# Optimization experiments

Hardware: AMD Instinct MI355X
Metric: run time of the kernel (lower is better)

The kernel has to match this reference:

```python
import jax, jax.numpy as jnp
import numpy as np

B, S, D, H = 8, 2048, 1024, 1024

def setup_inputs() -> dict:
    key = jax.random.key(0)
    ks = jax.random.split(key, 7)
    scale = 1.0 / np.sqrt(D)
    x = jax.random.normal(ks[0], (B, S, D), dtype=jnp.float32)
    W_q = jax.random.uniform(ks[1], (H, D), jnp.float32, -scale, scale)
    b_q = jax.random.uniform(ks[2], (H,), jnp.float32, -scale, scale)
    W_k = jax.random.uniform(ks[3], (H, D), jnp.float32, -scale, scale)
    b_k = jax.random.uniform(ks[4], (H,), jnp.float32, -scale, scale)
    W_v = jax.random.uniform(ks[5], (H, D), jnp.float32, -scale, scale)
    b_v = jax.random.uniform(ks[6], (H,), jnp.float32, -scale, scale)
    return {"x": x, "W_q": W_q, "b_q": b_q, "W_k": W_k, "b_k": b_k, "W_v": W_v, "b_v": b_v}

def reference(x, W_q, b_q, W_k, b_k, W_v, b_v):
    # Linear layers: y = x @ W.T + b (torch nn.Linear convention)
    q = jnp.einsum('bsd,hd->bsh', x, W_q) + b_q
    k = jnp.einsum('bsd,hd->bsh', x, W_k) + b_k
    v = jnp.einsum('bsd,hd->bsh', x, W_v) + b_v
    score = jnp.einsum('bqh,bkh->bqk', q, k) / jnp.sqrt(jnp.float32(H))
    causal = jnp.tril(jnp.ones((S, S), dtype=bool))  # lower-triangular mask
    score = jnp.where(causal, score, jnp.float32(-1e9))
    attn = jax.nn.softmax(score, axis=-1)
    return jnp.einsum('bqk,bkh->bqh', attn, v)
```

## Files before the change

kernel.cpp:

```cpp
#include <hip/hip_runtime.h>
#include <hip/hip_bf16.h>
#include <cstdint>

#define BB 8
#define SS 2048
#define DD 1024
#define HH 1024

typedef __bf16 bf16x8 __attribute__((ext_vector_type(8)));
typedef float f32x4 __attribute__((ext_vector_type(4)));

#define AS1C(p) ((const __attribute__((address_space(1))) void*)(p))
#define AS3(p)  ((__attribute__((address_space(3))) void*)(p))

__device__ __forceinline__ float bf2f(uint16_t h) {
  union { uint32_t u; float f; } v; v.u = ((uint32_t)h) << 16; return v.f;
}
__device__ __forceinline__ uint16_t f2bf(float f) {
  union { float f; uint32_t u; } v; v.f = f;
  uint32_t u = v.u;
  return (uint16_t)((u + 0x7FFFu + ((u >> 16) & 1u)) >> 16);
}

__global__ void cvt_f32_bf16(const float* __restrict__ src,
                             uint16_t* __restrict__ dst, int n) {
  int i = (blockIdx.x * blockDim.x + threadIdx.x) * 8;
  const int stride = gridDim.x * blockDim.x * 8;
  for (; i < n; i += stride) {
    float4 f0 = *(const float4*)(src + i);
    float4 f1 = *(const float4*)(src + i + 4);
    alignas(16) uint16_t o[8];
    o[0] = f2bf(f0.x); o[1] = f2bf(f0.y); o[2] = f2bf(f0.z); o[3] = f2bf(f0.w);
    o[4] = f2bf(f1.x); o[5] = f2bf(f1.y); o[6] = f2bf(f1.z); o[7] = f2bf(f1.w);
    *(uint4*)(dst + i) = *(const uint4*)o;
  }
}

__global__ void cvt3_f32_bf16(const float* __restrict__ s0, const float* __restrict__ s1,
                              const float* __restrict__ s2, uint16_t* __restrict__ d0,
                              uint16_t* __restrict__ d1, uint16_t* __restrict__ d2, int n) {
  const float* src = (blockIdx.y == 0) ? s0 : (blockIdx.y == 1) ? s1 : s2;
  uint16_t* dst = (blockIdx.y == 0) ? d0 : (blockIdx.y == 1) ? d1 : d2;
  int i = (blockIdx.x * blockDim.x + threadIdx.x) * 8;
  const int stride = gridDim.x * blockDim.x * 8;
  for (; i < n; i += stride) {
    float4 f0 = *(const float4*)(src + i);
    float4 f1 = *(const float4*)(src + i + 4);
    alignas(16) uint16_t o[8];
    o[0] = f2bf(f0.x); o[1] = f2bf(f0.y); o[2] = f2bf(f0.z); o[3] = f2bf(f0.w);
    o[4] = f2bf(f1.x); o[5] = f2bf(f1.y); o[6] = f2bf(f1.z); o[7] = f2bf(f1.w);
    *(uint4*)(dst + i) = *(const uint4*)o;
  }
}

template <int MODE>
__launch_bounds__(256, 2)
__global__ void gemm_bt(const uint16_t* __restrict__ Aroot,
                        const uint16_t* __restrict__ Broot,
                        const float* __restrict__ bq,
                        const float* __restrict__ bk,
                        const float* __restrict__ bv,
                        void* __restrict__ out0,
                        uint16_t* __restrict__ out1,
                        uint16_t* __restrict__ out2) {
  constexpr int K   = (MODE == 3) ? 2048 : 1024;
  constexpr int LDA = (MODE == 3) ? 2048 : 1024;
  constexpr int LDB = (MODE == 3) ? 2048 : 1024;

  const int tm = blockIdx.x, tn = blockIdx.y;
  if constexpr (MODE == 2) { if (tn > tm) return; }

  const uint16_t* A = Aroot;
  const uint16_t* Bp = Broot;
  uint16_t* C16 = (uint16_t*)out0;
  float*    C32 = (float*)out0;
  if constexpr (MODE == 2) {
    size_t z = blockIdx.z;
    A  += z * (size_t)(SS * DD);
    Bp += z * (size_t)(SS * DD);
    C16 += z * (size_t)SS * (size_t)SS;
  }
  if constexpr (MODE == 3) {
    size_t z = blockIdx.z;
    A  += z * (size_t)SS * (size_t)SS;
    Bp += z * (size_t)(HH * SS);
    C32 += z * (size_t)(SS * HH);
  }

  const int m0 = tm * 128, n0 = tn * 128;
  int kmax = K;
  if constexpr (MODE == 3) {
    kmax = (tm + 1) * 128;
    if (kmax > K) kmax = K;
  }

  __shared__ uint16_t As0[128 * 32];
  __shared__ uint16_t As1[128 * 32];
  __shared__ uint16_t Bs0[128 * 32];
  __shared__ uint16_t Bs1[128 * 32];

  const int tid  = threadIdx.x;
  const int lane = tid & 63;
  const int wv   = tid >> 6;
  const int wm   = (wv & 1) * 64;
  const int wn   = (wv >> 1) * 64;

  f32x4 acc[4][4];
#pragma unroll
  for (int i = 0; i < 4; i++)
#pragma unroll
    for (int j = 0; j < 4; j++)
#pragma unroll
      for (int e = 0; e < 4; e++) acc[i][j][e] = 0.f;

  const int lrow = lane >> 2;
  const int lcol = (lane & 3) * 8;
  const int r0   = wv * 32;

  const uint16_t* gA = A + (size_t)(m0 + r0 + lrow) * LDA + lcol;
  const uint16_t* gB = Bp + (size_t)(n0 + r0 + lrow) * LDB + lcol;

  const int fr = lane & 15;
  const int fk = (lane >> 4) * 8;

  for (int k0 = 0; k0 < kmax; k0 += 64) {
    __syncthreads();
    __builtin_amdgcn_global_load_lds(AS1C(gA + k0), AS3(&As0[r0 * 32]), 16, 0, 0);
    __builtin_amdgcn_global_load_lds(AS1C(gA + k0 + 16 * LDA), AS3(&As0[(r0 + 16) * 32]), 16, 0, 0);
    __builtin_amdgcn_global_load_lds(AS1C(gA + k0 + 32), AS3(&As1[r0 * 32]), 16, 0, 0);
    __builtin_amdgcn_global_load_lds(AS1C(gA + k0 + 32 + 16 * LDA), AS3(&As1[(r0 + 16) * 32]), 16, 0, 0);
    __builtin_amdgcn_global_load_lds(AS1C(gB + k0), AS3(&Bs0[r0 * 32]), 16, 0, 0);
    __builtin_amdgcn_global_load_lds(AS1C(gB + k0 + 16 * LDB), AS3(&Bs0[(r0 + 16) * 32]), 16, 0, 0);
    __builtin_amdgcn_global_load_lds(AS1C(gB + k0 + 32), AS3(&Bs1[r0 * 32]), 16, 0, 0);
    __builtin_amdgcn_global_load_lds(AS1C(gB + k0 + 32 + 16 * LDB), AS3(&Bs1[(r0 + 16) * 32]), 16, 0, 0);
    __syncthreads();

    bf16x8 af[4], bfr[4];
#pragma unroll
    for (int i = 0; i < 4; i++)
      af[i] = __builtin_bit_cast(bf16x8, *(const uint4*)&As0[(wm + i * 16 + fr) * 32 + fk]);
#pragma unroll
    for (int j = 0; j < 4; j++)
      bfr[j] = __builtin_bit_cast(bf16x8, *(const uint4*)&Bs0[(wn + j * 16 + fr) * 32 + fk]);
#pragma unroll
    for (int i = 0; i < 4; i++)
#pragma unroll
      for (int j = 0; j < 4; j++)
        acc[i][j] = __builtin_amdgcn_mfma_f32_16x16x32_bf16(af[i], bfr[j], acc[i][j], 0, 0, 0);

#pragma unroll
    for (int i = 0; i < 4; i++)
      af[i] = __builtin_bit_cast(bf16x8, *(const uint4*)&As1[(wm + i * 16 + fr) * 32 + fk]);
#pragma unroll
    for (int j = 0; j < 4; j++)
      bfr[j] = __builtin_bit_cast(bf16x8, *(const uint4*)&Bs1[(wn + j * 16 + fr) * 32 + fk]);
#pragma unroll
    for (int i = 0; i < 4; i++)
#pragma unroll
      for (int j = 0; j < 4; j++)
        acc[i][j] = __builtin_amdgcn_mfma_f32_16x16x32_bf16(af[i], bfr[j], acc[i][j], 0, 0, 0);
  }

  const int cr = (lane >> 4) * 4;
  const int cc = lane & 15;

  if constexpr (MODE == 0) {
    const int sel   = n0 >> 10;
    const int nloc0 = n0 & 1023;
    const float* __restrict__ bsel = (sel == 0) ? bq : (sel == 1) ? bk : bv;
    uint16_t* __restrict__ oQK = (sel == 1) ? out1 : (uint16_t*)out0;
#pragma unroll
    for (int i = 0; i < 4; i++) {
#pragma unroll
      for (int j = 0; j < 4; j++) {
        const int row0 = m0 + wm + i * 16 + cr;
        const int coll = nloc0 + wn + j * 16 + cc;
        const float badd = bsel[coll];
#pragma unroll
        for (int e = 0; e < 4; e++) {
          const float x = acc[i][j][e] + badd;
          const int r = row0 + e;
          if (sel == 2) {
            const int bz = r >> 11;
            const int s  = r & (SS - 1);
            out2[(size_t)bz * (HH * SS) + (size_t)coll * SS + s] = f2bf(x);
          } else {
            oQK[(size_t)r * HH + coll] = f2bf(x);
          }
        }
      }
    }
  } else {
#pragma unroll
    for (int i = 0; i < 4; i++) {
#pragma unroll
      for (int j = 0; j < 4; j++) {
        const int row0 = m0 + wm + i * 16 + cr;
        const int col  = n0 + wn + j * 16 + cc;
#pragma unroll
        for (int e = 0; e < 4; e++) {
          float x = acc[i][j][e];
          const int r = row0 + e;
          if constexpr (MODE == 2) {
            C16[(size_t)r * SS + col] = f2bf(x * 0.03125f);
          } else {
            C32[(size_t)r * HH + col] = x;
          }
        }
      }
    }
  }
}

__launch_bounds__(256)
__global__ void softmax_causal(uint16_t* __restrict__ Sb) {
  const int rgl = blockIdx.x;
  const int b = rgl >> 11;
  const int i = rgl & (SS - 1);
  uint16_t* row = Sb + (size_t)b * SS * SS + (size_t)i * SS;
  const int t = threadIdx.x;
  const int base = t * 8;

  uint4 u = *(const uint4*)(row + base);
  const uint16_t* hs = (const uint16_t*)&u;
  float x[8];
  float lmax = -3.0e38f;
#pragma unroll
  for (int e = 0; e < 8; e++) {
    float f = bf2f(hs[e]);
    x[e] = (base + e <= i) ? f : -3.0e38f;
    lmax = fmaxf(lmax, x[e]);
  }
#pragma unroll
  for (int off = 32; off > 0; off >>= 1)
    lmax = fmaxf(lmax, __shfl_down(lmax, off));

  __shared__ float red[8];
  if ((t & 63) == 0) red[t >> 6] = lmax;
  __syncthreads();
  const float m = fmaxf(fmaxf(red[0], red[1]), fmaxf(red[2], red[3]));

  float lsum = 0.f;
#pragma unroll
  for (int e = 0; e < 8; e++) {
    float p = (base + e <= i) ? __expf(x[e] - m) : 0.f;
    x[e] = p;
    lsum += p;
  }
#pragma unroll
  for (int off = 32; off > 0; off >>= 1) lsum += __shfl_down(lsum, off);
  if ((t & 63) == 0) red[4 + (t >> 6)] = lsum;
  __syncthreads();
  const float inv = 1.f / (red[4] + red[5] + red[6] + red[7]);

  alignas(16) uint16_t o[8];
#pragma unroll
  for (int e = 0; e < 8; e++) o[e] = f2bf(x[e] * inv);
  *(uint4*)(row + base) = *(const uint4*)o;
}

extern "C" void kernel_launch(void* const* d_in, const int* in_sizes, int n_in,
                              void* d_out, int out_size, void* d_ws, size_t ws_size,
                              hipStream_t stream) {
  const float* x  = (const float*)d_in[0];
  const float* Wq = (const float*)d_in[1];
  const float* bq = (const float*)d_in[2];
  const float* Wk = (const float*)d_in[3];
  const float* bk = (const float*)d_in[4];
  const float* Wv = (const float*)d_in[5];
  const float* bv = (const float*)d_in[6];

  uint16_t* ws = (uint16_t*)d_ws;
  const size_t QKV = (size_t)BB * SS * HH;
  uint16_t* Q  = ws;
  uint16_t* Kp = ws + QKV;
  uint16_t* Vt = ws + 2 * QKV;
  uint16_t* Sb = ws + 3 * QKV;
  uint16_t* xb  = Sb;
  uint16_t* Wqb = Sb + QKV;
  uint16_t* Wkb = Wqb + (size_t)HH * DD;
  uint16_t* Wvb = Wkb + (size_t)HH * DD;

  dim3 blk(256);
  const int nx = BB * SS * DD;
  const int nw = HH * DD;
  cvt_f32_bf16<<<dim3(nx / 2048), blk, 0, stream>>>(x, xb, nx);
  cvt3_f32_bf16<<<dim3(nw / 2048, 3), blk, 0, stream>>>(Wq, Wk, Wv, Wqb, Wkb, Wvb, nw);

  gemm_bt<0><<<dim3(BB * SS / 128, 3 * HH / 128), blk, 0, stream>>>(
      xb, Wqb, bq, bk, bv, Q, Kp, Vt);
  gemm_bt<2><<<dim3(SS / 128, SS / 128, BB), blk, 0, stream>>>(
      Q, Kp, nullptr, nullptr, nullptr, Sb, nullptr, nullptr);
  softmax_causal<<<dim3(BB * SS), blk, 0, stream>>>(Sb);
  gemm_bt<3><<<dim3(SS / 128, HH / 128, BB), blk, 0, stream>>>(
      Sb, Vt, nullptr, nullptr, nullptr, d_out, nullptr, nullptr);
}
```

Measured before the change: 424.0 us.

## Rewrite GEMM as 256x256 tile, 8-wave, double-buffered ping-pong pipeline with swizzled LDS

Replaces the 128x128 single-stage GEMM with a 256x256 tile computed by 512 threads (8 waves, each owning 128x64). K-tiles of 64 are double-buffered in LDS and prefetched with global_load_lds, interleaved with four MFMA quadrants separated by barriers and s_setprio. An XOR swizzle on the LDS column groups is meant to avoid bank conflicts. The goal is to hide global-load latency and raise MFMA utilisation. The cost is much more LDS (128 KB per block), heavier register pressure, fewer blocks per CU, and coarser causal work-skipping on the 256 granularity.

```diff
diff --git a/kernel.cpp b/kernel.cpp
--- a/kernel.cpp
+++ b/kernel.cpp
@@ -20,6 +20,12 @@
   union { float f; uint32_t u; } v; v.f = f;
   uint32_t u = v.u;
   return (uint16_t)((u + 0x7FFFu + ((u >> 16) & 1u)) >> 16);
+}
+
+__device__ __forceinline__ void wgbar() {
+  asm volatile("" ::: "memory");
+  __builtin_amdgcn_s_barrier();
+  asm volatile("" ::: "memory");
 }
 
 __global__ void cvt_f32_bf16(const float* __restrict__ src,
@@ -54,7 +60,7 @@
 }
 
 template <int MODE>
-__launch_bounds__(256, 2)
+__launch_bounds__(512, 2)
 __global__ void gemm_bt(const uint16_t* __restrict__ Aroot,
                         const uint16_t* __restrict__ Broot,
                         const float* __restrict__ bq,
@@ -70,95 +76,166 @@
   const int tm = blockIdx.x, tn = blockIdx.y;
   if constexpr (MODE == 2) { if (tn > tm) return; }
 
-  const uint16_t* A = Aroot;
+  const uint16_t* A  = Aroot;
   const uint16_t* Bp = Broot;
   uint16_t* C16 = (uint16_t*)out0;
   float*    C32 = (float*)out0;
   if constexpr (MODE == 2) {
     size_t z = blockIdx.z;
-    A  += z * (size_t)(SS * DD);
-    Bp += z * (size_t)(SS * DD);
+    A   += z * (size_t)(SS * DD);
+    Bp  += z * (size_t)(SS * DD);
     C16 += z * (size_t)SS * (size_t)SS;
   }
   if constexpr (MODE == 3) {
     size_t z = blockIdx.z;
-    A  += z * (size_t)SS * (size_t)SS;
-    Bp += z * (size_t)(HH * SS);
+    A   += z * (size_t)SS * (size_t)SS;
+    Bp  += z * (size_t)(HH * SS);
     C32 += z * (size_t)(SS * HH);
   }
 
-  const int m0 = tm * 128, n0 = tn * 128;
-  int kmax = K;
+  const int m0 = tm * 256, n0 = tn * 256;
+  int NT = K >> 6;
   if constexpr (MODE == 3) {
-    kmax = (tm + 1) * 128;
-    if (kmax > K) kmax = K;
-  }
-
-  __shared__ uint16_t As0[128 * 32];
-  __shared__ uint16_t As1[128 * 32];
-  __shared__ uint16_t Bs0[128 * 32];
-  __shared__ uint16_t Bs1[128 * 32];
+    int km = (tm + 1) * 256; if (km > K) km = K;
+    NT = km >> 6;
+  }
+
+  __shared__ uint16_t Al[2][256 * 64];
+  __shared__ uint16_t Bl[2][256 * 64];
 
   const int tid  = threadIdx.x;
   const int lane = tid & 63;
   const int wv   = tid >> 6;
-  const int wm   = (wv & 1) * 64;
-  const int wn   = (wv >> 1) * 64;
-
-  f32x4 acc[4][4];
-#pragma unroll
-  for (int i = 0; i < 4; i++)
+  const int wr   = wv >> 2;
+  const int wc   = wv & 3;
+
+  const int sr = lane >> 3;
+  const int sg = (lane & 7) ^ sr;
+  const uint16_t* gAs = A  + (size_t)m0 * LDA + (size_t)sr * LDA + sg * 8;
+  const uint16_t* gBs = Bp + (size_t)n0 * LDB + (size_t)sr * LDB + sg * 8;
+
+#define STAGE_A(BUF, H, K0)                                                    \
+  do {                                                                         \
+    __builtin_amdgcn_global_load_lds(                                          \
+        AS1C(gAs + (size_t)((H) * 128 + wv * 8) * LDA + (K0)),                 \
+        AS3(&Al[BUF][((H) * 128 + wv * 8) * 64]), 16, 0, 0);                   \
+    __builtin_amdgcn_global_load_lds(                                          \
+        AS1C(gAs + (size_t)((H) * 128 + 64 + wv * 8) * LDA + (K0)),            \
+        AS3(&Al[BUF][((H) * 128 + 64 + wv * 8) * 64]), 16, 0, 0);              \
+  } while (0)
+
+#define STAGE_B(BUF, H, K0)                                                    \
+  do {                                                                         \
+    __builtin_amdgcn_global_load_lds(                                          \
+        AS1C(gBs + (size_t)((H) * 128 + wv * 8) * LDB + (K0)),                 \
+        AS3(&Bl[BUF][((H) * 128 + wv * 8) * 64]), 16, 0, 0);                   \
+    __builtin_amdgcn_global_load_lds(                                          \
+        AS1C(gBs + (size_t)((H) * 128 + 64 + wv * 8) * LDB + (K0)),            \
+        AS3(&Bl[BUF][((H) * 128 + 64 + wv * 8) * 64]), 16, 0, 0);              \
+  } while (0)
+
+  const int rA  = lane & 15;
+  const int gk  = lane >> 4;
+  const int sw  = lane & 7;
+  const int ck0 = ((gk) ^ sw) * 8;
+  const int ck1 = ((4 + gk) ^ sw) * 8;
+  const int aro = (wr * 128 + rA) * 64;
+  const int bro = (wc * 64 + rA) * 64;
+
+  f32x4 acc[8][4];
+#pragma unroll
+  for (int i = 0; i < 8; i++)
 #pragma unroll
     for (int j = 0; j < 4; j++)
 #pragma unroll
       for (int e = 0; e < 4; e++) acc[i][j][e] = 0.f;
 
-  const int lrow = lane >> 2;
-  const int lcol = (lane & 3) * 8;
-  const int r0   = wv * 32;
-
-  const uint16_t* gA = A + (size_t)(m0 + r0 + lrow) * LDA + lcol;
-  const uint16_t* gB = Bp + (size_t)(n0 + r0 + lrow) * LDB + lcol;
-
-  const int fr = lane & 15;
-  const int fk = (lane >> 4) * 8;
-
-  for (int k0 = 0; k0 < kmax; k0 += 64) {
-    __syncthreads();
-    __builtin_amdgcn_global_load_lds(AS1C(gA + k0), AS3(&As0[r0 * 32]), 16, 0, 0);
-    __builtin_amdgcn_global_load_lds(AS1C(gA + k0 + 16 * LDA), AS3(&As0[(r0 + 16) * 32]), 16, 0, 0);
-    __builtin_amdgcn_global_load_lds(AS1C(gA + k0 + 32), AS3(&As1[r0 * 32]), 16, 0, 0);
-    __builtin_amdgcn_global_load_lds(AS1C(gA + k0 + 32 + 16 * LDA), AS3(&As1[(r0 + 16) * 32]), 16, 0, 0);
-    __builtin_amdgcn_global_load_lds(AS1C(gB + k0), AS3(&Bs0[r0 * 32]), 16, 0, 0);
-    __builtin_amdgcn_global_load_lds(AS1C(gB + k0 + 16 * LDB), AS3(&Bs0[(r0 + 16) * 32]), 16, 0, 0);
-    __builtin_amdgcn_global_load_lds(AS1C(gB + k0 + 32), AS3(&Bs1[r0 * 32]), 16, 0, 0);
-    __builtin_amdgcn_global_load_lds(AS1C(gB + k0 + 32 + 16 * LDB), AS3(&Bs1[(r0 + 16) * 32]), 16, 0, 0);
-    __syncthreads();
-
-    bf16x8 af[4], bfr[4];
-#pragma unroll
-    for (int i = 0; i < 4; i++)
-      af[i] = __builtin_bit_cast(bf16x8, *(const uint4*)&As0[(wm + i * 16 + fr) * 32 + fk]);
-#pragma unroll
-    for (int j = 0; j < 4; j++)
-      bfr[j] = __builtin_bit_cast(bf16x8, *(const uint4*)&Bs0[(wn + j * 16 + fr) * 32 + fk]);
-#pragma unroll
-    for (int i = 0; i < 4; i++)
-#pragma unroll
-      for (int j = 0; j < 4; j++)
-        acc[i][j] = __builtin_amdgcn_mfma_f32_16x16x32_bf16(af[i], bfr[j], acc[i][j], 0, 0, 0);
-
-#pragma unroll
-    for (int i = 0; i < 4; i++)
-      af[i] = __builtin_bit_cast(bf16x8, *(const uint4*)&As1[(wm + i * 16 + fr) * 32 + fk]);
-#pragma unroll
-    for (int j = 0; j < 4; j++)
-      bfr[j] = __builtin_bit_cast(bf16x8, *(const uint4*)&Bs1[(wn + j * 16 + fr) * 32 + fk]);
-#pragma unroll
-    for (int i = 0; i < 4; i++)
-#pragma unroll
-      for (int j = 0; j < 4; j++)
-        acc[i][j] = __builtin_amdgcn_mfma_f32_16x16x32_bf16(af[i], bfr[j], acc[i][j], 0, 0, 0);
+  bf16x8 af[4][2], bfj[4][2];
+
+#define LDF(BASE, OFF) __builtin_bit_cast(bf16x8, *(const uint4*)&(BASE)[OFF])
+
+#define QUAD(MH, JH)                                                           \
+  do {                                                                         \
+    _Pragma("unroll") for (int i = 0; i < 4; ++i)                              \
+    _Pragma("unroll") for (int j = 0; j < 2; ++j) {                            \
+      acc[(MH)*4 + i][(JH)*2 + j] = __builtin_amdgcn_mfma_f32_16x16x32_bf16(   \
+          af[i][0], bfj[(JH)*2 + j][0], acc[(MH)*4 + i][(JH)*2 + j], 0, 0, 0); \
+      acc[(MH)*4 + i][(JH)*2 + j] = __builtin_amdgcn_mfma_f32_16x16x32_bf16(   \
+          af[i][1], bfj[(JH)*2 + j][1], acc[(MH)*4 + i][(JH)*2 + j], 0, 0, 0); \
+    }                                                                          \
+  } while (0)
+
+  STAGE_A(0, 0, 0); STAGE_A(0, 1, 0);
+  STAGE_B(0, 0, 0); STAGE_B(0, 1, 0);
+  if (NT > 1) {
+    STAGE_B(1, 0, 64); STAGE_B(1, 1, 64);
+    STAGE_A(1, 0, 64);
+    asm volatile("s_waitcnt vmcnt(6)" ::: "memory");
+  } else {
+    asm volatile("s_waitcnt vmcnt(0)" ::: "memory");
+  }
+  wgbar();
+
+  for (int t = 0; t < NT; ++t) {
+    const int c = t & 1;
+    const uint16_t* Ab = Al[c];
+    const uint16_t* Bb = Bl[c];
+    const int kc = t * 64;
+
+#pragma unroll
+    for (int i = 0; i < 4; ++i) {
+      af[i][0] = LDF(Ab, aro + (i * 16) * 64 + ck0);
+      af[i][1] = LDF(Ab, aro + (i * 16) * 64 + ck1);
+    }
+#pragma unroll
+    for (int j = 0; j < 2; ++j) {
+      bfj[j][0] = LDF(Bb, bro + (j * 16) * 64 + ck0);
+      bfj[j][1] = LDF(Bb, bro + (j * 16) * 64 + ck1);
+    }
+    if (t + 1 < NT) STAGE_A(c ^ 1, 1, kc + 64);
+    wgbar();
+    asm volatile("s_waitcnt lgkmcnt(0)" ::: "memory");
+    __builtin_amdgcn_s_setprio(1);
+    QUAD(0, 0);
+    __builtin_amdgcn_s_setprio(0);
+    wgbar();
+
+#pragma unroll
+    for (int j = 2; j < 4; ++j) {
+      bfj[j][0] = LDF(Bb, bro + (j * 16) * 64 + ck0);
+      bfj[j][1] = LDF(Bb, bro + (j * 16) * 64 + ck1);
+    }
+    wgbar();
+    asm volatile("s_waitcnt lgkmcnt(0)" ::: "memory");
+    __builtin_amdgcn_s_setprio(1);
+    QUAD(0, 1);
+    __builtin_amdgcn_s_setprio(0);
+    wgbar();
+
+#pragma unroll
+    for (int i = 0; i < 4; ++i) {
+      af[i][0] = LDF(Ab, aro + ((64 + i * 16)) * 64 + ck0);
+      af[i][1] = LDF(Ab, aro + ((64 + i * 16)) * 64 + ck1);
+    }
+    if (t + 2 < NT) { STAGE_B(c, 0, kc + 128); STAGE_B(c, 1, kc + 128); }
+    wgbar();
+    asm volatile("s_waitcnt lgkmcnt(0)" ::: "memory");
+    __builtin_amdgcn_s_setprio(1);
+    QUAD(1, 0);
+    __builtin_amdgcn_s_setprio(0);
+    wgbar();
+
+    if (t + 2 < NT) STAGE_A(c, 0, kc + 128);
+    wgbar();
+    __builtin_amdgcn_s_setprio(1);
+    QUAD(1, 1);
+    __builtin_amdgcn_s_setprio(0);
+    if (t + 2 < NT) {
+      asm volatile("s_waitcnt vmcnt(6)" ::: "memory");
+    } else if (t + 1 < NT) {
+      asm volatile("s_waitcnt vmcnt(0)" ::: "memory");
+    }
+    wgbar();
   }
 
   const int cr = (lane >> 4) * 4;
@@ -170,11 +247,11 @@
     const float* __restrict__ bsel = (sel == 0) ? bq : (sel == 1) ? bk : bv;
     uint16_t* __restrict__ oQK = (sel == 1) ? out1 : (uint16_t*)out0;
 #pragma unroll
-    for (int i = 0; i < 4; i++) {
+    for (int i = 0; i < 8; i++) {
 #pragma unroll
       for (int j = 0; j < 4; j++) {
-        const int row0 = m0 + wm + i * 16 + cr;
-        const int coll = nloc0 + wn + j * 16 + cc;
+        const int row0 = m0 + wr * 128 + i * 16 + cr;
+        const int coll = nloc0 + wc * 64 + j * 16 + cc;
         const float badd = bsel[coll];
 #pragma unroll
         for (int e = 0; e < 4; e++) {
@@ -192,11 +269,11 @@
     }
   } else {
 #pragma unroll
-    for (int i = 0; i < 4; i++) {
+    for (int i = 0; i < 8; i++) {
 #pragma unroll
       for (int j = 0; j < 4; j++) {
-        const int row0 = m0 + wm + i * 16 + cr;
-        const int col  = n0 + wn + j * 16 + cc;
+        const int row0 = m0 + wr * 128 + i * 16 + cr;
+        const int col  = n0 + wc * 64 + j * 16 + cc;
 #pragma unroll
         for (int e = 0; e < 4; e++) {
           float x = acc[i][j][e];
@@ -210,6 +287,10 @@
       }
     }
   }
+#undef STAGE_A
+#undef STAGE_B
+#undef LDF
+#undef QUAD
 }
 
 __launch_bounds__(256)
@@ -282,16 +363,17 @@
   uint16_t* Wvb = Wkb + (size_t)HH * DD;
 
   dim3 blk(256);
+  dim3 blk512(512);
   const int nx = BB * SS * DD;
   const int nw = HH * DD;
   cvt_f32_bf16<<<dim3(nx / 2048), blk, 0, stream>>>(x, xb, nx);
   cvt3_f32_bf16<<<dim3(nw / 2048, 3), blk, 0, stream>>>(Wq, Wk, Wv, Wqb, Wkb, Wvb, nw);
 
-  gemm_bt<0><<<dim3(BB * SS / 128, 3 * HH / 128), blk, 0, stream>>>(
+  gemm_bt<0><<<dim3(BB * SS / 256, 3 * HH / 256), blk512, 0, stream>>>(
       xb, Wqb, bq, bk, bv, Q, Kp, Vt);
-  gemm_bt<2><<<dim3(SS / 128, SS / 128, BB), blk, 0, stream>>>(
+  gemm_bt<2><<<dim3(SS / 256, SS / 256, BB), blk512, 0, stream>>>(
       Q, Kp, nullptr, nullptr, nullptr, Sb, nullptr, nullptr);
   softmax_causal<<<dim3(BB * SS), blk, 0, stream>>>(Sb);
-  gemm_bt<3><<<dim3(SS / 128, HH / 128, BB), blk, 0, stream>>>(
+  gemm_bt<3><<<dim3(SS / 256, HH / 256, BB), blk512, 0, stream>>>(
       Sb, Vt, nullptr, nullptr, nullptr, d_out, nullptr, nullptr);
 }
```

After: 437.6 us. +3.2%, slower.
